# Kernel optimization log

Hardware: AMD Instinct MI355X
Metric: run time of the kernel (lower is better)

## Reference

```python
import jax, jax.numpy as jnp
import numpy as np

B, S, D, H = 2, 2048, 2048, 16
DH = D // H  # 128
MAX_SEQ = 2048


def _rope_tables(dim, max_seq_len):
    inv_freq = 1.0 / (10000.0 ** (jnp.arange(0, dim, 2, dtype=jnp.float32) / dim))
    t = jnp.arange(max_seq_len, dtype=jnp.float32)
    freqs = jnp.einsum('i,j->ij', t, inv_freq)          # [S, dim/2]
    emb = jnp.concatenate([freqs, freqs], axis=-1)       # [S, dim]
    return jnp.cos(emb), jnp.sin(emb)


def setup_inputs() -> dict:
    key = jax.random.key(0)
    kx, kq, kk, kv, ko = jax.random.split(key, 5)
    scale = 1.0 / np.sqrt(D)
    x = jax.random.normal(kx, (B, S, D), dtype=jnp.float32)
    # nn.Linear weights: [out_features, in_features], y = x @ W.T
    wq = jax.random.normal(kq, (H * DH, D), dtype=jnp.float32) * scale
    wk = jax.random.normal(kk, (H * DH, D), dtype=jnp.float32) * scale
    wv = jax.random.normal(kv, (H * DH, D), dtype=jnp.float32) * scale
    wo = jax.random.normal(ko, (D, H * DH), dtype=jnp.float32) * scale
    cos, sin = _rope_tables(DH, MAX_SEQ)
    return {"x": x, "wq": wq, "wk": wk, "wv": wv, "wo": wo,
            "cos": cos, "sin": sin}


def _rotate(t):
    # faithful to torch: cat([-t[..., 1::2], t[..., ::2]], dim=-1)
    return jnp.concatenate([-t[..., 1::2], t[..., ::2]], axis=-1)


def reference(x, wq, wk, wv, wo, cos, sin):
    b, s, _ = x.shape
    # QKV projections -> [b, h, s, dh]
    def proj(w):
        return jnp.einsum('bsd,ed->bse', x, w).reshape(b, s, H, DH).transpose(0, 2, 1, 3)
    q, k, v = proj(wq), proj(wk), proj(wv)
    c = cos[:s, :]  # [s, dh], broadcasts over b, h
    si = sin[:s, :]
    q = q * c + _rotate(q) * si
    k = k * c + _rotate(k) * si
    # scaled dot-product attention, non-causal
    scores = jnp.einsum('bhqd,bhkd->bhqk', q, k) / np.sqrt(DH)
    attn = jax.nn.softmax(scores, axis=-1)
    out = jnp.einsum('bhqk,bhkd->bhqd', attn, v)
    out = out.transpose(0, 2, 1, 3).reshape(b, s, H * DH)
    return jnp.einsum('bse,de->bsd', out, wo)
```

## Files before the change

kernel.cpp:

```cpp
#include <hip/hip_runtime.h>

#define SQ   2048
#define DIMD 2048
#define NH   16
#define HD   128
#define MR   4096
#define QBLK 128
#define KBLK 64

using u16 = unsigned short;
using u32 = unsigned int;
using s16x8 = __attribute__((ext_vector_type(8))) short;
using u16x8 = __attribute__((ext_vector_type(8))) unsigned short;
using f32x4 = __attribute__((ext_vector_type(4))) float;
using as3u  = __attribute__((address_space(3))) u32;
using as1u  = __attribute__((address_space(1))) u32;

__device__ __forceinline__ u16 f2bf(float f) {
  u32 x = __float_as_uint(f);
  return (u16)((x + 0x7fffu + ((x >> 16) & 1u)) >> 16);
}
__device__ __forceinline__ float bf2f(u16 u) {
  return __uint_as_float(((u32)u) << 16);
}
__device__ __forceinline__ void gld16(const void* g, void* l) {
  __builtin_amdgcn_global_load_lds((as1u*)g, (as3u*)l, 16, 0, 0);
}
#define MFMA16 __builtin_amdgcn_mfma_f32_16x16x32_bf16

__global__ __launch_bounds__(256) void cvt_bf16(const float* __restrict__ s,
                                                u16* __restrict__ d, int n4) {
  int i = blockIdx.x * 256 + threadIdx.x;
  int st = gridDim.x * 256;
  for (; i < n4; i += st) {
    float4 v = ((const float4*)s)[i];
    u32 lo = (u32)f2bf(v.x) | ((u32)f2bf(v.y) << 16);
    u32 hi = (u32)f2bf(v.z) | ((u32)f2bf(v.w) << 16);
    ((uint2*)d)[i] = make_uint2(lo, hi);
  }
}

__global__ __launch_bounds__(256) void cvt_w4(const float* __restrict__ w0,
                                              const float* __restrict__ w1,
                                              const float* __restrict__ w2,
                                              const float* __restrict__ w3,
                                              u16* __restrict__ d) {
  const int n4 = DIMD * DIMD / 4;
  int y = blockIdx.y;
  const float* s = (y == 0) ? w0 : (y == 1) ? w1 : (y == 2) ? w2 : w3;
  u16* dst = d + (size_t)y * DIMD * DIMD;
  int i = blockIdx.x * 256 + threadIdx.x;
  int st = gridDim.x * 256;
  for (; i < n4; i += st) {
    float4 v = ((const float4*)s)[i];
    u32 lo = (u32)f2bf(v.x) | ((u32)f2bf(v.y) << 16);
    u32 hi = (u32)f2bf(v.z) | ((u32)f2bf(v.w) << 16);
    ((uint2*)dst)[i] = make_uint2(lo, hi);
  }
}

__global__ __launch_bounds__(256) void rope_kernel(
    const u16* __restrict__ Qin, const u16* __restrict__ Kin,
    u16* __restrict__ Qout, u16* __restrict__ Kout,
    const float* __restrict__ cosT, const float* __restrict__ sinT) {
  int ten = blockIdx.y;
  const u16* in = ten ? Kin : Qin;
  u16* outp     = ten ? Kout : Qout;
  float scl     = ten ? 1.0f : 0.08838834764831845f;
  int row = blockIdx.x * 4 + (threadIdx.x >> 6);
  int j   = threadIdx.x & 63;
  int s   = row & (SQ - 1);
  const u16* r = in + (size_t)row * HD;
  u16* w = outp + (size_t)row * HD;
  float c  = cosT[s * HD + j];
  float si = sinT[s * HD + j];
  float a  = bf2f(r[j]);
  float b  = bf2f(r[j + 64]);
  float ev = bf2f(r[2 * j]);
  float od = bf2f(r[2 * j + 1]);
  w[j]      = f2bf((a * c - od * si) * scl);
  w[j + 64] = f2bf((b * c + ev * si) * scl);
}

template <int MODE>
__global__ __launch_bounds__(256) void gemm_bt(
    const u16* __restrict__ A,
    const u16* __restrict__ W0, const u16* __restrict__ W1, const u16* __restrict__ W2,
    u16* __restrict__ O0, u16* __restrict__ O1, u16* __restrict__ O2,
    float* __restrict__ Ofp) {
  __shared__ alignas(16) u16 SM[17408];
  u16* lA = SM;
  u16* lB = SM + 8192;
  int t = threadIdx.x;
  int l = t & 63, l15 = l & 15, lg = l >> 4;
  int wid = t >> 6, wr = wid >> 1, wc = wid & 1;
  int mi = blockIdx.x >> 4, ni = blockIdx.x & 15;
  int m0 = mi * 128, n0 = ni * 128;
  const u16* W = W0;
  u16* Ob = O0;
  if (MODE == 0) {
    if (blockIdx.y == 1) { W = W1; Ob = O1; }
    else if (blockIdx.y == 2) { W = W2; Ob = O2; }
  }
  const u16* Ag = A + (size_t)m0 * DIMD;
  const u16* Wg = W + (size_t)n0 * DIMD;
  int r0 = t >> 2, ch = (t & 3) * 8;

  f32x4 acc[4][4];
#pragma unroll
  for (int a1 = 0; a1 < 4; a1++)
#pragma unroll
    for (int b1 = 0; b1 < 4; b1++) acc[a1][b1] = (f32x4){0.f, 0.f, 0.f, 0.f};

  auto stage = [&](int buf, int kb) {
    int k0 = kb * 32;
    gld16(Ag + (size_t)r0 * DIMD + k0 + ch,        &lA[buf * 4096 + t * 8]);
    gld16(Ag + (size_t)(r0 + 64) * DIMD + k0 + ch, &lA[buf * 4096 + (t + 256) * 8]);
    gld16(Wg + (size_t)r0 * DIMD + k0 + ch,        &lB[buf * 4096 + t * 8]);
    gld16(Wg + (size_t)(r0 + 64) * DIMD + k0 + ch, &lB[buf * 4096 + (t + 256) * 8]);
  };

  stage(0, 0);
  __syncthreads();
#pragma unroll 2
  for (int kb = 0; kb < DIMD / 32; kb++) {
    if (kb + 1 < DIMD / 32) stage((kb + 1) & 1, kb + 1);
    int buf = kb & 1;
    s16x8 af[4], bfr[4];
#pragma unroll
    for (int rb = 0; rb < 4; rb++)
      af[rb] = *(const s16x8*)&lA[buf * 4096 + (wr * 64 + rb * 16 + l15) * 32 + lg * 8];
#pragma unroll
    for (int cb = 0; cb < 4; cb++)
      bfr[cb] = *(const s16x8*)&lB[buf * 4096 + (wc * 64 + cb * 16 + l15) * 32 + lg * 8];
#pragma unroll
    for (int rb = 0; rb < 4; rb++)
#pragma unroll
      for (int cb = 0; cb < 4; cb++)
        acc[rb][cb] = MFMA16(af[rb], bfr[cb], acc[rb][cb], 0, 0, 0);
    __syncthreads();
  }

  if (MODE == 0 && blockIdx.y == 2) {
    u16 (*lT)[132] = (u16(*)[132])SM;
#pragma unroll
    for (int rb = 0; rb < 4; rb++)
#pragma unroll
      for (int cb = 0; cb < 4; cb++)
#pragma unroll
        for (int i = 0; i < 4; i++)
          lT[wr * 64 + rb * 16 + lg * 4 + i][wc * 64 + cb * 16 + l15] =
              f2bf(acc[rb][cb][i]);
    __syncthreads();
    int b = m0 >> 11, s0 = m0 & (SQ - 1), h = n0 >> 7;
    int dh = t >> 1, sc = (t & 1) * 64;
    u16* dst = Ob + ((size_t)(b * NH + h) * HD + dh) * SQ + s0 + sc;
#pragma unroll
    for (int c8 = 0; c8 < 8; c8++) {
      u16x8 o;
#pragma unroll
      for (int e = 0; e < 8; e++) o[e] = lT[sc + c8 * 8 + e][dh];
      *(u16x8*)(dst + c8 * 8) = o;
    }
    return;
  }

#pragma unroll
  for (int rb = 0; rb < 4; rb++) {
#pragma unroll
    for (int cb = 0; cb < 4; cb++) {
#pragma unroll
      for (int i = 0; i < 4; i++) {
        float v = acc[rb][cb][i];
        int mm = m0 + wr * 64 + rb * 16 + lg * 4 + i;
        int nn = n0 + wc * 64 + cb * 16 + l15;
        if (MODE == 0) {
          int b = mm >> 11, s2 = mm & (SQ - 1), h = nn >> 7, dh = nn & (HD - 1);
          Ob[((size_t)(b * NH + h) * SQ + s2) * HD + dh] = f2bf(v);
        } else {
          Ofp[(size_t)mm * DIMD + nn] = v;
        }
      }
    }
  }
}

__global__ __launch_bounds__(256, 2) void attn_kernel(
    const u16* __restrict__ Q, const u16* __restrict__ K,
    const u16* __restrict__ Vt, u16* __restrict__ Aout) {
  __shared__ alignas(16) u16 Ksh[2][KBLK * HD];
  __shared__ alignas(16) u16 Vsh[2][HD * KBLK];
  __shared__ alignas(16) u16 Pl[4][32 * KBLK];
  int t = threadIdx.x;
  int wid = t >> 6, l = t & 63, l15 = l & 15, lg = l >> 4;
  int orig = blockIdx.x;
  int bid = (orig & 7) * 64 + (orig >> 3);
  int qb = bid & 15, bh = bid >> 4;
  int q0 = qb * QBLK + wid * 32;
  const u16* Qb = Q + ((size_t)bh * SQ + q0) * HD;
  const u16* Kb = K + (size_t)bh * SQ * HD;
  const u16* Vb = Vt + (size_t)bh * HD * SQ;

  s16x8 qf[2][4];
#pragma unroll
  for (int mq = 0; mq < 2; mq++)
#pragma unroll
    for (int ks = 0; ks < 4; ks++)
      qf[mq][ks] = *(const s16x8*)(Qb + (size_t)(mq * 16 + l15) * HD + ks * 32 + lg * 8);

  int od[4], kro[4], kco[4], vro[4], vco[4];
#pragma unroll
  for (int p2 = 0; p2 < 4; p2++) {
    int off = t * 16 + p2 * 4096;
    od[p2] = off;
    kro[p2] = off >> 8; kco[p2] = (off & 255) ^ ((kro[p2] & 7) << 4);
    vro[p2] = off >> 7; vco[p2] = (off & 127) ^ ((vro[p2] & 7) << 4);
  }

  auto stage = [&](int buf, int kb) {
    const u16* Kt = Kb + (size_t)kb * KBLK * HD;
    const u16* Vs = Vb + kb * KBLK;
#pragma unroll
    for (int p2 = 0; p2 < 4; p2++)
      gld16(Kt + (size_t)kro[p2] * HD + (kco[p2] >> 1), &Ksh[buf][od[p2] >> 1]);
#pragma unroll
    for (int p2 = 0; p2 < 4; p2++)
      gld16(Vs + (size_t)vro[p2] * SQ + (vco[p2] >> 1), &Vsh[buf][od[p2] >> 1]);
  };

  f32x4 acc[2][8];
#pragma unroll
  for (int mq = 0; mq < 2; mq++)
#pragma unroll
    for (int i = 0; i < 8; i++) acc[mq][i] = (f32x4){0.f, 0.f, 0.f, 0.f};
  float m[2] = {-3.0e38f, -3.0e38f}, lsum[2] = {0.f, 0.f};

  stage(0, 0);
  __syncthreads();

#pragma unroll 1
  for (int kb = 0; kb < SQ / KBLK; kb++) {
    int cur = kb & 1;
    if (kb + 1 < SQ / KBLK) stage(cur ^ 1, kb + 1);
    f32x4 sa[2][4];
#pragma unroll
    for (int mq = 0; mq < 2; mq++)
#pragma unroll
      for (int cb = 0; cb < 4; cb++) sa[mq][cb] = (f32x4){0.f, 0.f, 0.f, 0.f};
    __builtin_amdgcn_s_setprio(1);
#pragma unroll
    for (int ks = 0; ks < 4; ks++) {
#pragma unroll
      for (int cb = 0; cb < 4; cb++) {
        int r = cb * 16 + l15;
        int off = r * 256 + ((ks * 64 + lg * 16) ^ ((r & 7) << 4));
        s16x8 kf = *(const s16x8*)((const char*)&Ksh[cur][0] + off);
        sa[0][cb] = MFMA16(kf, qf[0][ks], sa[0][cb], 0, 0, 0);
        sa[1][cb] = MFMA16(kf, qf[1][ks], sa[1][cb], 0, 0, 0);
      }
    }
    __builtin_amdgcn_s_setprio(0);
    float rm[2];
#pragma unroll
    for (int mq = 0; mq < 2; mq++) {
      float r2 = sa[mq][0][0];
#pragma unroll
      for (int cb = 0; cb < 4; cb++)
#pragma unroll
        for (int i = 0; i < 4; i++) r2 = fmaxf(r2, sa[mq][cb][i]);
      r2 = fmaxf(r2, __shfl_xor(r2, 16));
      r2 = fmaxf(r2, __shfl_xor(r2, 32));
      rm[mq] = r2;
    }
    if (!__all(rm[0] <= m[0] + 8.0f && rm[1] <= m[1] + 8.0f)) {
#pragma unroll
      for (int mq = 0; mq < 2; mq++) {
        float mn = fmaxf(m[mq], rm[mq]);
        float al = __expf(m[mq] - mn);
        m[mq] = mn;
        float alq[4];
#pragma unroll
        for (int i = 0; i < 4; i++) alq[i] = __shfl(al, lg * 4 + i, 16);
#pragma unroll
        for (int c2 = 0; c2 < 8; c2++)
#pragma unroll
          for (int i = 0; i < 4; i++) acc[mq][c2][i] *= alq[i];
        lsum[mq] *= al;
      }
    }
#pragma unroll
    for (int mq = 0; mq < 2; mq++) {
      float ps = 0.f;
#pragma unroll
      for (int cb = 0; cb < 4; cb++)
#pragma unroll
        for (int i = 0; i < 4; i++) {
          sa[mq][cb][i] = __expf(sa[mq][cb][i] - m[mq]);
          ps += sa[mq][cb][i];
        }
      ps += __shfl_xor(ps, 16);
      ps += __shfl_xor(ps, 32);
      lsum[mq] += ps;
    }
#pragma unroll
    for (int mq = 0; mq < 2; mq++)
#pragma unroll
      for (int cb = 0; cb < 4; cb++) {
        u32 lo = (u32)f2bf(sa[mq][cb][0]) | ((u32)f2bf(sa[mq][cb][1]) << 16);
        u32 hi = (u32)f2bf(sa[mq][cb][2]) | ((u32)f2bf(sa[mq][cb][3]) << 16);
        int off = (mq * 16 + l15) * 128 + ((cb * 32 + lg * 8) ^ ((l15 & 7) << 4));
        *(uint2*)((char*)&Pl[wid][0] + off) = make_uint2(lo, hi);
      }
    s16x8 pf[2][2];
#pragma unroll
    for (int mq = 0; mq < 2; mq++)
#pragma unroll
      for (int k2 = 0; k2 < 2; k2++) {
        int off = (mq * 16 + l15) * 128 + ((k2 * 64 + lg * 16) ^ ((l15 & 7) << 4));
        pf[mq][k2] = *(const s16x8*)((const char*)&Pl[wid][0] + off);
      }
    __builtin_amdgcn_s_setprio(1);
#pragma unroll
    for (int c2 = 0; c2 < 8; c2++) {
#pragma unroll
      for (int k2 = 0; k2 < 2; k2++) {
        int r = c2 * 16 + l15;
        int off = r * 128 + ((k2 * 64 + lg * 16) ^ ((r & 7) << 4));
        s16x8 vf = *(const s16x8*)((const char*)&Vsh[cur][0] + off);
        acc[0][c2] = MFMA16(pf[0][k2], vf, acc[0][c2], 0, 0, 0);
        acc[1][c2] = MFMA16(pf[1][k2], vf, acc[1][c2], 0, 0, 0);
      }
    }
    __builtin_amdgcn_s_setprio(0);
    __syncthreads();
  }
  int b = bh >> 4, h = bh & (NH - 1);
#pragma unroll
  for (int mq = 0; mq < 2; mq++) {
    float rin = 1.0f / lsum[mq];
    float rq[4];
#pragma unroll
    for (int i = 0; i < 4; i++) rq[i] = __shfl(rin, lg * 4 + i, 16);
#pragma unroll
    for (int c2 = 0; c2 < 8; c2++) {
#pragma unroll
      for (int i = 0; i < 4; i++) {
        int q = q0 + mq * 16 + lg * 4 + i;
        int dh = c2 * 16 + l15;
        Aout[((size_t)b * SQ + q) * DIMD + h * HD + dh] = f2bf(acc[mq][c2][i] * rq[i]);
      }
    }
  }
}

extern "C" void kernel_launch(void* const* d_in, const int* in_sizes, int n_in,
                              void* d_out, int out_size, void* d_ws, size_t ws_size,
                              hipStream_t stream) {
  (void)in_sizes; (void)n_in; (void)out_size; (void)ws_size;
  const float* x    = (const float*)d_in[0];
  const float* wq   = (const float*)d_in[1];
  const float* wk   = (const float*)d_in[2];
  const float* wv   = (const float*)d_in[3];
  const float* wo   = (const float*)d_in[4];
  const float* cosT = (const float*)d_in[5];
  const float* sinT = (const float*)d_in[6];
  float* out = (float*)d_out;

  char* p = (char*)d_ws;
  const size_t SZ_MD = (size_t)MR * DIMD * 2;
  const size_t SZ_W  = (size_t)DIMD * DIMD * 2;
  u16* xb   = (u16*)p; p += SZ_MD;
  u16* wqb  = (u16*)p; p += SZ_W;
  u16* wkb  = (u16*)p; p += SZ_W;
  u16* wvb  = (u16*)p; p += SZ_W;
  u16* wob  = (u16*)p; p += SZ_W;
  u16* Qraw = (u16*)p; p += SZ_MD;
  u16* Kraw = (u16*)p; p += SZ_MD;
  u16* Qr   = (u16*)p; p += SZ_MD;
  u16* Kr   = (u16*)p; p += SZ_MD;
  u16* Vt   = (u16*)p; p += SZ_MD;
  u16* attnout = Qraw;

  cvt_bf16<<<1024, 256, 0, stream>>>(x, xb, MR * DIMD / 4);
  cvt_w4<<<dim3(512, 4), 256, 0, stream>>>(wq, wk, wv, wo, wqb);

  gemm_bt<0><<<dim3(512, 3), 256, 0, stream>>>(xb, wqb, wkb, wvb, Qraw, Kraw, Vt, nullptr);
  rope_kernel<<<dim3(16384, 2), 256, 0, stream>>>(Qraw, Kraw, Qr, Kr, cosT, sinT);
  attn_kernel<<<512, 256, 0, stream>>>(Qr, Kr, Vt, attnout);
  gemm_bt<1><<<dim3(512, 1), 256, 0, stream>>>(attnout, wob, nullptr, nullptr,
                                               nullptr, nullptr, nullptr, out);
}
```

Baseline: 311.3 us.

## Fuse RoPE into Q/K projection GEMM epilogue and split V GEMM

The RoPE rotation and Q scaling now run in the epilogue of the Q/K projection GEMM, working from the LDS-staged output tile, so the separate rope kernel and the raw Q/K buffers are gone. This removes one write and one read of the full Q and K tensors plus a kernel launch. V gets its own GEMM kernel that keeps the transposed-store epilogue. The output GEMM becomes a specialised kernel, and the epilogue now does strided LDS reads and per-element cos/sin loads.

New measurement: 436.1 us. +40.1%, slower.

```diff
diff --git a/kernel.cpp b/kernel.cpp
--- a/kernel.cpp
+++ b/kernel.cpp
@@ -59,130 +59,132 @@
   }
 }
 
-__global__ __launch_bounds__(256) void rope_kernel(
-    const u16* __restrict__ Qin, const u16* __restrict__ Kin,
-    u16* __restrict__ Qout, u16* __restrict__ Kout,
+#define GEMM_CORE(Ag_, Wg_)                                                    \
+  int t = threadIdx.x;                                                         \
+  int l = t & 63, l15 = l & 15, lg = l >> 4;                                   \
+  int wid = t >> 6, wr = wid >> 1, wc = wid & 1;                               \
+  int mi = blockIdx.x >> 4, ni = blockIdx.x & 15;                              \
+  int m0 = mi * 128, n0 = ni * 128;                                            \
+  const u16* Ag = (Ag_) + (size_t)m0 * DIMD;                                   \
+  const u16* Wg = (Wg_) + (size_t)n0 * DIMD;                                   \
+  int r0 = t >> 2, ch = (t & 3) * 8;                                           \
+  f32x4 acc[4][4];                                                             \
+  _Pragma("unroll") for (int a1 = 0; a1 < 4; a1++)                             \
+      _Pragma("unroll") for (int b1 = 0; b1 < 4; b1++)                         \
+          acc[a1][b1] = (f32x4){0.f, 0.f, 0.f, 0.f};                           \
+  auto stage = [&](int buf, int kb) {                                          \
+    int k0 = kb * 32;                                                          \
+    gld16(Ag + (size_t)r0 * DIMD + k0 + ch,        &lA[buf * 4096 + t * 8]);   \
+    gld16(Ag + (size_t)(r0 + 64) * DIMD + k0 + ch, &lA[buf * 4096 + (t + 256) * 8]); \
+    gld16(Wg + (size_t)r0 * DIMD + k0 + ch,        &lB[buf * 4096 + t * 8]);   \
+    gld16(Wg + (size_t)(r0 + 64) * DIMD + k0 + ch, &lB[buf * 4096 + (t + 256) * 8]); \
+  };                                                                           \
+  stage(0, 0);                                                                 \
+  __syncthreads();                                                             \
+  _Pragma("unroll 2") for (int kb = 0; kb < DIMD / 32; kb++) {                 \
+    if (kb + 1 < DIMD / 32) stage((kb + 1) & 1, kb + 1);                       \
+    int buf = kb & 1;                                                          \
+    s16x8 af[4], bfr[4];                                                       \
+    _Pragma("unroll") for (int rb = 0; rb < 4; rb++)                           \
+        af[rb] = *(const s16x8*)&lA[buf * 4096 + (wr * 64 + rb * 16 + l15) * 32 + lg * 8]; \
+    _Pragma("unroll") for (int cb = 0; cb < 4; cb++)                           \
+        bfr[cb] = *(const s16x8*)&lB[buf * 4096 + (wc * 64 + cb * 16 + l15) * 32 + lg * 8]; \
+    _Pragma("unroll") for (int rb = 0; rb < 4; rb++)                           \
+        _Pragma("unroll") for (int cb = 0; cb < 4; cb++)                       \
+            acc[rb][cb] = MFMA16(af[rb], bfr[cb], acc[rb][cb], 0, 0, 0);       \
+    __syncthreads();                                                           \
+  }
+
+__global__ __launch_bounds__(256) void gemm_qk(
+    const u16* __restrict__ A, const u16* __restrict__ W0, const u16* __restrict__ W1,
+    u16* __restrict__ O0, u16* __restrict__ O1,
     const float* __restrict__ cosT, const float* __restrict__ sinT) {
-  int ten = blockIdx.y;
-  const u16* in = ten ? Kin : Qin;
-  u16* outp     = ten ? Kout : Qout;
-  float scl     = ten ? 1.0f : 0.08838834764831845f;
-  int row = blockIdx.x * 4 + (threadIdx.x >> 6);
-  int j   = threadIdx.x & 63;
-  int s   = row & (SQ - 1);
-  const u16* r = in + (size_t)row * HD;
-  u16* w = outp + (size_t)row * HD;
-  float c  = cosT[s * HD + j];
-  float si = sinT[s * HD + j];
-  float a  = bf2f(r[j]);
-  float b  = bf2f(r[j + 64]);
-  float ev = bf2f(r[2 * j]);
-  float od = bf2f(r[2 * j + 1]);
-  w[j]      = f2bf((a * c - od * si) * scl);
-  w[j + 64] = f2bf((b * c + ev * si) * scl);
-}
-
-template <int MODE>
-__global__ __launch_bounds__(256) void gemm_bt(
-    const u16* __restrict__ A,
-    const u16* __restrict__ W0, const u16* __restrict__ W1, const u16* __restrict__ W2,
-    u16* __restrict__ O0, u16* __restrict__ O1, u16* __restrict__ O2,
-    float* __restrict__ Ofp) {
   __shared__ alignas(16) u16 SM[17408];
   u16* lA = SM;
   u16* lB = SM + 8192;
-  int t = threadIdx.x;
-  int l = t & 63, l15 = l & 15, lg = l >> 4;
-  int wid = t >> 6, wr = wid >> 1, wc = wid & 1;
-  int mi = blockIdx.x >> 4, ni = blockIdx.x & 15;
-  int m0 = mi * 128, n0 = ni * 128;
-  const u16* W = W0;
-  u16* Ob = O0;
-  if (MODE == 0) {
-    if (blockIdx.y == 1) { W = W1; Ob = O1; }
-    else if (blockIdx.y == 2) { W = W2; Ob = O2; }
-  }
-  const u16* Ag = A + (size_t)m0 * DIMD;
-  const u16* Wg = W + (size_t)n0 * DIMD;
-  int r0 = t >> 2, ch = (t & 3) * 8;
-
-  f32x4 acc[4][4];
-#pragma unroll
-  for (int a1 = 0; a1 < 4; a1++)
-#pragma unroll
-    for (int b1 = 0; b1 < 4; b1++) acc[a1][b1] = (f32x4){0.f, 0.f, 0.f, 0.f};
-
-  auto stage = [&](int buf, int kb) {
-    int k0 = kb * 32;
-    gld16(Ag + (size_t)r0 * DIMD + k0 + ch,        &lA[buf * 4096 + t * 8]);
-    gld16(Ag + (size_t)(r0 + 64) * DIMD + k0 + ch, &lA[buf * 4096 + (t + 256) * 8]);
-    gld16(Wg + (size_t)r0 * DIMD + k0 + ch,        &lB[buf * 4096 + t * 8]);
-    gld16(Wg + (size_t)(r0 + 64) * DIMD + k0 + ch, &lB[buf * 4096 + (t + 256) * 8]);
-  };
-
-  stage(0, 0);
+  const u16* Wsel = blockIdx.y ? W1 : W0;
+  u16* Ob = blockIdx.y ? O1 : O0;
+  float scl = blockIdx.y ? 1.0f : 0.08838834764831845f;
+  GEMM_CORE(A, Wsel)
+  u16 (*lT)[132] = (u16(*)[132])SM;
+#pragma unroll
+  for (int rb = 0; rb < 4; rb++)
+#pragma unroll
+    for (int cb = 0; cb < 4; cb++)
+#pragma unroll
+      for (int i = 0; i < 4; i++)
+        lT[wr * 64 + rb * 16 + lg * 4 + i][wc * 64 + cb * 16 + l15] =
+            f2bf(acc[rb][cb][i]);
   __syncthreads();
-#pragma unroll 2
-  for (int kb = 0; kb < DIMD / 32; kb++) {
-    if (kb + 1 < DIMD / 32) stage((kb + 1) & 1, kb + 1);
-    int buf = kb & 1;
-    s16x8 af[4], bfr[4];
-#pragma unroll
-    for (int rb = 0; rb < 4; rb++)
-      af[rb] = *(const s16x8*)&lA[buf * 4096 + (wr * 64 + rb * 16 + l15) * 32 + lg * 8];
+  int b = m0 >> 11, h = n0 >> 7;
+  int r = t & 127, half = t >> 7;
+  int s = (m0 + r) & (SQ - 1);
+  const float* cT = cosT + s * HD + half * 64;
+  const float* sT = sinT + s * HD + half * 64;
+  u16* dst = Ob + ((size_t)(b * NH + h) * SQ + s) * HD + half * 64;
+#pragma unroll
+  for (int c8 = 0; c8 < 8; c8++) {
+    u16x8 o;
+#pragma unroll
+    for (int e = 0; e < 8; e++) {
+      int j = c8 * 8 + e;
+      float c = cT[j], si = sT[j];
+      float v;
+      if (half == 0) v = bf2f(lT[r][j]) * c - bf2f(lT[r][2 * j + 1]) * si;
+      else           v = bf2f(lT[r][64 + j]) * c + bf2f(lT[r][2 * j]) * si;
+      o[e] = f2bf(v * scl);
+    }
+    *(u16x8*)(dst + c8 * 8) = o;
+  }
+}
+
+__global__ __launch_bounds__(256) void gemm_v(
+    const u16* __restrict__ A, const u16* __restrict__ W,
+    u16* __restrict__ Ob) {
+  __shared__ alignas(16) u16 SM[17408];
+  u16* lA = SM;
+  u16* lB = SM + 8192;
+  GEMM_CORE(A, W)
+  u16 (*lT)[132] = (u16(*)[132])SM;
+#pragma unroll
+  for (int rb = 0; rb < 4; rb++)
 #pragma unroll
     for (int cb = 0; cb < 4; cb++)
-      bfr[cb] = *(const s16x8*)&lB[buf * 4096 + (wc * 64 + cb * 16 + l15) * 32 + lg * 8];
-#pragma unroll
-    for (int rb = 0; rb < 4; rb++)
-#pragma unroll
-      for (int cb = 0; cb < 4; cb++)
-        acc[rb][cb] = MFMA16(af[rb], bfr[cb], acc[rb][cb], 0, 0, 0);
-    __syncthreads();
-  }
-
-  if (MODE == 0 && blockIdx.y == 2) {
-    u16 (*lT)[132] = (u16(*)[132])SM;
-#pragma unroll
-    for (int rb = 0; rb < 4; rb++)
-#pragma unroll
-      for (int cb = 0; cb < 4; cb++)
-#pragma unroll
-        for (int i = 0; i < 4; i++)
-          lT[wr * 64 + rb * 16 + lg * 4 + i][wc * 64 + cb * 16 + l15] =
-              f2bf(acc[rb][cb][i]);
-    __syncthreads();
-    int b = m0 >> 11, s0 = m0 & (SQ - 1), h = n0 >> 7;
-    int dh = t >> 1, sc = (t & 1) * 64;
-    u16* dst = Ob + ((size_t)(b * NH + h) * HD + dh) * SQ + s0 + sc;
-#pragma unroll
-    for (int c8 = 0; c8 < 8; c8++) {
-      u16x8 o;
-#pragma unroll
-      for (int e = 0; e < 8; e++) o[e] = lT[sc + c8 * 8 + e][dh];
-      *(u16x8*)(dst + c8 * 8) = o;
-    }
-    return;
-  }
-
-#pragma unroll
-  for (int rb = 0; rb < 4; rb++) {
-#pragma unroll
-    for (int cb = 0; cb < 4; cb++) {
+#pragma unroll
+      for (int i = 0; i < 4; i++)
+        lT[wr * 64 + rb * 16 + lg * 4 + i][wc * 64 + cb * 16 + l15] =
+            f2bf(acc[rb][cb][i]);
+  __syncthreads();
+  int b = m0 >> 11, s0 = m0 & (SQ - 1), h = n0 >> 7;
+  int dh = t >> 1, sc = (t & 1) * 64;
+  u16* dst = Ob + ((size_t)(b * NH + h) * HD + dh) * SQ + s0 + sc;
+#pragma unroll
+  for (int c8 = 0; c8 < 8; c8++) {
+    u16x8 o;
+#pragma unroll
+    for (int e = 0; e < 8; e++) o[e] = lT[sc + c8 * 8 + e][dh];
+    *(u16x8*)(dst + c8 * 8) = o;
+  }
+}
+
+__global__ __launch_bounds__(256) void gemm_o(
+    const u16* __restrict__ A, const u16* __restrict__ W,
+    float* __restrict__ Ofp) {
+  __shared__ alignas(16) u16 lAb[2][4096];
+  __shared__ alignas(16) u16 lBb[2][4096];
+  u16* lA = &lAb[0][0];
+  u16* lB = &lBb[0][0];
+  GEMM_CORE(A, W)
+#pragma unroll
+  for (int rb = 0; rb < 4; rb++)
+#pragma unroll
+    for (int cb = 0; cb < 4; cb++)
 #pragma unroll
       for (int i = 0; i < 4; i++) {
-        float v = acc[rb][cb][i];
         int mm = m0 + wr * 64 + rb * 16 + lg * 4 + i;
         int nn = n0 + wc * 64 + cb * 16 + l15;
-        if (MODE == 0) {
-          int b = mm >> 11, s2 = mm & (SQ - 1), h = nn >> 7, dh = nn & (HD - 1);
-          Ob[((size_t)(b * NH + h) * SQ + s2) * HD + dh] = f2bf(v);
-        } else {
-          Ofp[(size_t)mm * DIMD + nn] = v;
-        }
-      }
-    }
-  }
+        Ofp[(size_t)mm * DIMD + nn] = acc[rb][cb][i];
+      }
 }
 
 __global__ __launch_bounds__(256, 2) void attn_kernel(
@@ -374,19 +376,16 @@
   u16* wkb  = (u16*)p; p += SZ_W;
   u16* wvb  = (u16*)p; p += SZ_W;
   u16* wob  = (u16*)p; p += SZ_W;
-  u16* Qraw = (u16*)p; p += SZ_MD;
-  u16* Kraw = (u16*)p; p += SZ_MD;
   u16* Qr   = (u16*)p; p += SZ_MD;
   u16* Kr   = (u16*)p; p += SZ_MD;
   u16* Vt   = (u16*)p; p += SZ_MD;
-  u16* attnout = Qraw;
+  u16* attnout = (u16*)p; p += SZ_MD;
 
   cvt_bf16<<<1024, 256, 0, stream>>>(x, xb, MR * DIMD / 4);
   cvt_w4<<<dim3(512, 4), 256, 0, stream>>>(wq, wk, wv, wo, wqb);
 
-  gemm_bt<0><<<dim3(512, 3), 256, 0, stream>>>(xb, wqb, wkb, wvb, Qraw, Kraw, Vt, nullptr);
-  rope_kernel<<<dim3(16384, 2), 256, 0, stream>>>(Qraw, Kraw, Qr, Kr, cosT, sinT);
+  gemm_qk<<<dim3(512, 2), 256, 0, stream>>>(xb, wqb, wkb, Qr, Kr, cosT, sinT);
+  gemm_v<<<512, 256, 0, stream>>>(xb, wvb, Vt);
   attn_kernel<<<512, 256, 0, stream>>>(Qr, Kr, Vt, attnout);
-  gemm_bt<1><<<dim3(512, 1), 256, 0, stream>>>(attnout, wob, nullptr, nullptr,
-                                               nullptr, nullptr, nullptr, out);
-}
+  gemm_o<<<512, 256, 0, stream>>>(attnout, wob, out);
+}
```
